# Kernel tuning notes

Hardware: AMD Instinct MI355X
Metric: run time of the kernel (lower is better)

Reference implementation:

```python
import jax, jax.numpy as jnp
import numpy as np
import math

HIDDEN = 1024
HEADS = 16
HEAD_DIM = HIDDEN // HEADS


def setup_inputs() -> dict:
    key = jax.random.key(0)
    ks = jax.random.split(key, 9)
    s = 1.0 / math.sqrt(HIDDEN)
    x = jax.random.normal(ks[0], (4, 2048, HIDDEN), dtype=jnp.float32)
    Wq = jax.random.uniform(ks[1], (HIDDEN, HIDDEN), jnp.float32, -s, s)
    bq = jax.random.uniform(ks[2], (HIDDEN,), jnp.float32, -s, s)
    Wk = jax.random.uniform(ks[3], (HIDDEN, HIDDEN), jnp.float32, -s, s)
    bk = jax.random.uniform(ks[4], (HIDDEN,), jnp.float32, -s, s)
    Wv = jax.random.uniform(ks[5], (HIDDEN, HIDDEN), jnp.float32, -s, s)
    bv = jax.random.uniform(ks[6], (HIDDEN,), jnp.float32, -s, s)
    Wo = jax.random.uniform(ks[7], (HIDDEN, HIDDEN), jnp.float32, -s, s)
    bo = jax.random.uniform(ks[8], (HIDDEN,), jnp.float32, -s, s)
    return {"x": x, "Wq": Wq, "bq": bq, "Wk": Wk, "bk": bk,
            "Wv": Wv, "bv": bv, "Wo": Wo, "bo": bo}


def reference(x, Wq, bq, Wk, bk, Wv, bv, Wo, bo):
    B, T, D = x.shape
    H, Hd = HEADS, HEAD_DIM
    scale = 1.0 / math.sqrt(Hd)
    # projections (torch Linear: y = x @ W.T + b)
    q = (x @ Wq.T + bq).reshape(B, T, H, Hd).transpose(0, 2, 1, 3)  # [B,H,T,Hd]
    k = (x @ Wk.T + bk).reshape(B, T, H, Hd).transpose(0, 2, 1, 3)
    v = (x @ Wv.T + bv).reshape(B, T, H, Hd).transpose(0, 2, 1, 3)
    scores = jnp.einsum("bhqd,bhkd->bhqk", q, k) * scale  # [B,H,T,T]
    attn = jax.nn.softmax(scores, axis=-1)
    out = jnp.einsum("bhqk,bhkd->bhqd", attn, v)  # [B,H,T,Hd]
    out = out.transpose(0, 2, 1, 3).reshape(B, T, D)
    out = out @ Wo.T + bo
    return out.mean(axis=1)  # [B, D]
```

## Files before the change

### kernel.cpp

```cpp
#include <hip/hip_runtime.h>
#include <stdint.h>

#define HIDDEN 1024
#define HEADS 16
#define HEAD_DIM 64
#define BATCH 4
#define SEQ 2048
#define NTOK (BATCH * SEQ)

typedef __attribute__((ext_vector_type(8))) short bf16x8;
typedef __attribute__((ext_vector_type(4))) float floatx4;
typedef __attribute__((ext_vector_type(16))) float floatx16;

#define SCALE_Q 0.18033688011112042f

__device__ __forceinline__ unsigned short f2bf(float f) {
    union { float f; unsigned u; } x; x.f = f;
    unsigned r = x.u + 0x7fffu + ((x.u >> 16) & 1u);
    return (unsigned short)(r >> 16);
}

__device__ __forceinline__ float fast_exp2(float x) {
#if __has_builtin(__builtin_amdgcn_exp2f)
    return __builtin_amdgcn_exp2f(x);
#else
    return exp2f(x);
#endif
}

typedef __attribute__((address_space(3))) unsigned int lds_u32;
typedef const __attribute__((address_space(1))) unsigned int gl_u32;

__device__ __forceinline__ void async_cp16(const void* g, void* l) {
#if __has_builtin(__builtin_amdgcn_global_load_lds)
    __builtin_amdgcn_global_load_lds((gl_u32*)g, (lds_u32*)l, 16, 0, 0);
#else
    *(uint4*)((char*)l + (threadIdx.x & 63) * 16) = *(const uint4*)g;
#endif
}

__global__ __launch_bounds__(256) void conv_all(
    const float* __restrict__ x, const float* __restrict__ Wq,
    const float* __restrict__ Wk, const float* __restrict__ Wv,
    unsigned short* __restrict__ x_bf, unsigned short* __restrict__ wq_bf,
    unsigned short* __restrict__ wk_bf, unsigned short* __restrict__ wv_bf,
    float* __restrict__ accp) {
    const int blk = blockIdx.x, tid = threadIdx.x;
    const float* src;
    unsigned short* dst;
    size_t i;
    if (blk < 8192) {
        src = x; dst = x_bf; i = (size_t)blk * 256 + tid;
        if (blk < 16) accp[blk * 256 + tid] = 0.0f;
    } else {
        int r = blk - 8192;
        int s = r >> 10;
        src = (s == 0) ? Wq : (s == 1) ? Wk : Wv;
        dst = (s == 0) ? wq_bf : (s == 1) ? wk_bf : wv_bf;
        i = (size_t)(r & 1023) * 256 + tid;
    }
    float4 v = *(const float4*)(src + 4 * i);
    unsigned short o[4];
    o[0] = f2bf(v.x); o[1] = f2bf(v.y); o[2] = f2bf(v.z); o[3] = f2bf(v.w);
    *(ushort4*)(dst + 4 * i) = *(ushort4*)o;
}

__global__ __launch_bounds__(256, 3) void qkv_gemm(
    const unsigned short* __restrict__ X,
    const unsigned short* __restrict__ W0, const unsigned short* __restrict__ W1,
    const unsigned short* __restrict__ W2,
    const float* __restrict__ b0, const float* __restrict__ b1,
    const float* __restrict__ b2,
    unsigned short* __restrict__ O0, unsigned short* __restrict__ O1,
    unsigned short* __restrict__ O2) {
    __shared__ unsigned short Alds[2][4096];
    __shared__ unsigned short Blds[2][4096];

    const int id = blockIdx.x;
    const int y = id >> 6;
    const int z = y >> 3;
    const int n0 = (y & 7) * 128;
    const int m0 = (id & 63) * 128;
    const unsigned short* W = (z == 0) ? W0 : (z == 1) ? W1 : W2;
    const float* bias       = (z == 0) ? b0 : (z == 1) ? b1 : b2;
    unsigned short* O       = (z == 0) ? O0 : (z == 1) ? O1 : O2;

    const int tid = threadIdx.x, lane = tid & 63, wave = tid >> 6;
    const int mw = (wave >> 1) * 64, nw = (wave & 1) * 64;

    const int sr = lane >> 2;
    const int scb = (lane & 3) * 8;
    const unsigned short* ga[2];
    const unsigned short* gb[2];
#pragma unroll
    for (int j = 0; j < 2; ++j) {
        ga[j] = X + (size_t)(m0 + wave * 32 + j * 16 + sr) * HIDDEN + scb;
        gb[j] = W + (size_t)(n0 + wave * 32 + j * 16 + sr) * HIDDEN + scb;
    }

    floatx4 acc[4][4];
#pragma unroll
    for (int tm = 0; tm < 4; ++tm)
#pragma unroll
        for (int tn = 0; tn < 4; ++tn)
#pragma unroll
            for (int r = 0; r < 4; ++r) acc[tm][tn][r] = 0.f;

#pragma unroll
    for (int j = 0; j < 2; ++j) {
        async_cp16(ga[j], (char*)Alds[0] + wave * 2048 + j * 1024);
        async_cp16(gb[j], (char*)Blds[0] + wave * 2048 + j * 1024);
        ga[j] += 32; gb[j] += 32;
    }
    __syncthreads();

    const int frag_off = (lane & 15) * 64 + (lane >> 4) * 16;
    for (int kt = 0; kt < 32; ++kt) {
        const int cur = kt & 1;
        if (kt < 31) {
#pragma unroll
            for (int j = 0; j < 2; ++j) {
                async_cp16(ga[j], (char*)Alds[cur ^ 1] + wave * 2048 + j * 1024);
                async_cp16(gb[j], (char*)Blds[cur ^ 1] + wave * 2048 + j * 1024);
                ga[j] += 32; gb[j] += 32;
            }
        }
        bf16x8 af[4], bfr[4];
#pragma unroll
        for (int t = 0; t < 4; ++t) {
            af[t]  = *(bf16x8*)((char*)Alds[cur] + (mw + t * 16) * 64 + frag_off);
            bfr[t] = *(bf16x8*)((char*)Blds[cur] + (nw + t * 16) * 64 + frag_off);
        }
#pragma unroll
        for (int tm = 0; tm < 4; ++tm)
#pragma unroll
            for (int tn = 0; tn < 4; ++tn)
                acc[tm][tn] = __builtin_amdgcn_mfma_f32_16x16x32_bf16(af[tm], bfr[tn], acc[tm][tn], 0, 0, 0);
        if (kt < 31) __syncthreads();
    }

    const int col = lane & 15, rbase = (lane >> 4) * 4;
#pragma unroll
    for (int tm = 0; tm < 4; ++tm) {
#pragma unroll
        for (int tn = 0; tn < 4; ++tn) {
            const int n = n0 + nw + tn * 16 + col;
            const float bs = bias[n];
            const int m_base = m0 + mw + tm * 16 + rbase;
            if (z == 2) {
                const int hh = n >> 6, dd = n & 63;
                const int bb = m_base >> 11, tt = m_base & (SEQ - 1);
                unsigned short vals[4];
#pragma unroll
                for (int r = 0; r < 4; ++r) vals[r] = f2bf(acc[tm][tn][r] + bs);
                *(ushort4*)&O[(((size_t)bb * HEADS + hh) * HEAD_DIM + dd) * SEQ + tt] = *(ushort4*)vals;
            } else {
                const float sc = (z == 0) ? SCALE_Q : 1.0f;
#pragma unroll
                for (int r = 0; r < 4; ++r)
                    O[(size_t)(m_base + r) * HIDDEN + n] = f2bf((acc[tm][tn][r] + bs) * sc);
            }
        }
    }
}

__global__ __launch_bounds__(256, 2) void attn_mfma(
    const unsigned short* __restrict__ Q, const unsigned short* __restrict__ K,
    const unsigned short* __restrict__ Vt, float* __restrict__ accp) {
    __shared__ unsigned short Klds[2][8192];
    __shared__ unsigned short Vlds[2][8192];

    const int tid = threadIdx.x, lane = tid & 63, wave = tid >> 6;
    const int lq = lane & 31, g2 = lane >> 5;

    const int f = blockIdx.x;
    const int bh = (f & 7) * 8 + ((f >> 3) & 7);
    const int qc = f >> 6;
    const int b = bh >> 4, h = bh & 15;

    bf16x8 qfrag[2][4];
#pragma unroll
    for (int g = 0; g < 2; ++g) {
        const size_t qb = ((size_t)(b * SEQ + qc * 256 + wave * 64 + g * 32 + lq)) * HIDDEN
                          + h * HEAD_DIM + g2 * 8;
#pragma unroll
        for (int ds = 0; ds < 4; ++ds) qfrag[g][ds] = *(const bf16x8*)&Q[qb + ds * 16];
    }

    const unsigned short* kg[4];
    const unsigned short* vg[4];
    {
        const int kr = lane >> 3;
        const int kc = ((lane & 7) ^ kr) * 8;
#pragma unroll
        for (int j = 0; j < 4; ++j)
            kg[j] = K + ((size_t)(b * SEQ + wave * 32 + j * 8 + kr)) * HIDDEN + h * HEAD_DIM + kc;
#pragma unroll
        for (int j = 0; j < 4; ++j) {
            const int dl = wave * 16 + j * 4 + (lane >> 4);
            const int cc = ((lane & 15) ^ (dl & 15)) * 8;
            vg[j] = Vt + ((size_t)bh * HEAD_DIM + dl) * SEQ + cc;
        }
    }

    floatx16 oacc[2][2], lacc[2];
#pragma unroll
    for (int g = 0; g < 2; ++g)
#pragma unroll
        for (int r = 0; r < 16; ++r) { oacc[g][0][r] = 0.f; oacc[g][1][r] = 0.f; lacc[g][r] = 0.f; }

    bf16x8 ones;
    {
        union { bf16x8 v; unsigned u[4]; } o;
        o.u[0] = o.u[1] = o.u[2] = o.u[3] = 0x3F803F80u;
        ones = o.v;
    }

#pragma unroll
    for (int j = 0; j < 4; ++j) {
        async_cp16(kg[j], (char*)Klds[0] + (wave * 32 + j * 8) * 128);
        async_cp16(vg[j], (char*)Vlds[0] + (wave * 16 + j * 4) * 256);
        kg[j] += 128 * HIDDEN; vg[j] += 128;
    }
    __syncthreads();

    for (int it = 0; it < 16; ++it) {
        const int cur = it & 1;
        if (it < 15) {
#pragma unroll
            for (int j = 0; j < 4; ++j) {
                async_cp16(kg[j], (char*)Klds[cur ^ 1] + (wave * 32 + j * 8) * 128);
                async_cp16(vg[j], (char*)Vlds[cur ^ 1] + (wave * 16 + j * 4) * 256);
                kg[j] += 128 * HIDDEN; vg[j] += 128;
            }
        }
#pragma unroll
        for (int ks4 = 0; ks4 < 4; ++ks4) {
            const int kk = ks4 * 32;
            const int rr = kk + lq;
            bf16x8 kf[4];
#pragma unroll
            for (int ds = 0; ds < 4; ++ds)
                kf[ds] = *(bf16x8*)((char*)Klds[cur] + rr * 128 + (((g2 + 2 * ds) ^ (lq & 7)) * 16));

            unsigned pk[2][8];
#pragma unroll
            for (int g = 0; g < 2; ++g) {
                floatx16 sacc;
#pragma unroll
                for (int r = 0; r < 16; ++r) sacc[r] = 0.f;
#pragma unroll
                for (int ds = 0; ds < 4; ++ds)
                    sacc = __builtin_amdgcn_mfma_f32_32x32x16_bf16(kf[ds], qfrag[g][ds], sacc, 0, 0, 0);
#pragma unroll
                for (int j = 0; j < 8; ++j) {
                    union { float f; unsigned u; } plo, phi;
                    plo.f = fast_exp2(sacc[2 * j]);
                    phi.f = fast_exp2(sacc[2 * j + 1]);
                    pk[g][j] = __builtin_amdgcn_perm(phi.u, plo.u, 0x07060302u);
                }
            }
#pragma unroll
            for (int ks2 = 0; ks2 < 2; ++ks2) {
                bf16x8 vf[2];
#pragma unroll
                for (int nf = 0; nf < 2; ++nf) {
                    const int d = nf * 32 + lq;
                    const int c0 = (4 * ks4 + 2 * ks2) ^ (d & 15);
                    const int c1 = (4 * ks4 + 2 * ks2 + 1) ^ (d & 15);
                    union { uint2 h[2]; bf16x8 v; } u;
                    u.h[0] = *(uint2*)((char*)Vlds[cur] + d * 256 + c0 * 16 + g2 * 8);
                    u.h[1] = *(uint2*)((char*)Vlds[cur] + d * 256 + c1 * 16 + g2 * 8);
                    vf[nf] = u.v;
                }
#pragma unroll
                for (int g = 0; g < 2; ++g) {
                    union { uint4 u; bf16x8 v; } af;
                    af.u.x = pk[g][4 * ks2];
                    af.u.y = pk[g][4 * ks2 + 1];
                    af.u.z = pk[g][4 * ks2 + 2];
                    af.u.w = pk[g][4 * ks2 + 3];
#pragma unroll
                    for (int nf = 0; nf < 2; ++nf)
                        oacc[g][nf] = __builtin_amdgcn_mfma_f32_32x32x16_bf16(af.v, vf[nf], oacc[g][nf], 0, 0, 0);
                    lacc[g] = __builtin_amdgcn_mfma_f32_32x32x16_bf16(af.v, ones, lacc[g], 0, 0, 0);
                }
            }
        }
        if (it < 15) __syncthreads();
    }

#pragma unroll
    for (int g = 0; g < 2; ++g)
#pragma unroll
        for (int nf = 0; nf < 2; ++nf) {
            float v = 0.f;
#pragma unroll
            for (int r = 0; r < 16; ++r) v += oacc[g][nf][r] / lacc[g][r];
            v += __shfl_xor(v, 32, 64);
            if (lane < 32)
                atomicAdd(&accp[b * HIDDEN + h * HEAD_DIM + nf * 32 + lq], v);
        }
}

__global__ __launch_bounds__(256) void out_proj(const float* __restrict__ acc,
                                                const float* __restrict__ Wo,
                                                const float* __restrict__ bo,
                                                float* __restrict__ out) {
    const int n = blockIdx.x * 256 + threadIdx.x;
    const int b = blockIdx.y;
    const float invT = 1.0f / (float)SEQ;
    float s = 0.f;
    for (int k = 0; k < HIDDEN; k += 4) {
        float4 w = *(const float4*)&Wo[(size_t)n * HIDDEN + k];
        float4 a = *(const float4*)&acc[b * HIDDEN + k];
        s += w.x * a.x + w.y * a.y + w.z * a.z + w.w * a.w;
    }
    out[b * HIDDEN + n] = s * invT + bo[n];
}

extern "C" void kernel_launch(void* const* d_in, const int* in_sizes, int n_in,
                              void* d_out, int out_size, void* d_ws, size_t ws_size,
                              hipStream_t stream) {
    const float* x  = (const float*)d_in[0];
    const float* Wq = (const float*)d_in[1];
    const float* bq = (const float*)d_in[2];
    const float* Wk = (const float*)d_in[3];
    const float* bk = (const float*)d_in[4];
    const float* Wv = (const float*)d_in[5];
    const float* bv = (const float*)d_in[6];
    const float* Wo = (const float*)d_in[7];
    const float* bo = (const float*)d_in[8];
    float* out = (float*)d_out;

    char* ws = (char*)d_ws;
    unsigned short* x_bf  = (unsigned short*)(ws);
    unsigned short* wq_bf = (unsigned short*)(ws + 16777216);
    unsigned short* wk_bf = (unsigned short*)(ws + 18874368);
    unsigned short* wv_bf = (unsigned short*)(ws + 20971520);
    unsigned short* q_bf  = (unsigned short*)(ws + 23068672);
    unsigned short* k_bf  = (unsigned short*)(ws + 39845888);
    unsigned short* vt_bf = (unsigned short*)(ws + 56623104);
    float*          accp  = (float*)(ws + 73400320);

    conv_all<<<dim3(8192 + 3072), dim3(256), 0, stream>>>(
        x, Wq, Wk, Wv, x_bf, wq_bf, wk_bf, wv_bf, accp);

    qkv_gemm<<<dim3(64 * 24), dim3(256), 0, stream>>>(
        x_bf, wq_bf, wk_bf, wv_bf, bq, bk, bv, q_bf, k_bf, vt_bf);

    attn_mfma<<<dim3(512), dim3(256), 0, stream>>>(q_bf, k_bf, vt_bf, accp);

    out_proj<<<dim3(HIDDEN / 256, BATCH), dim3(256), 0, stream>>>(accp, Wo, bo, out);
}
```

Before: 266.2 us.

## Swizzle GEMM LDS, stage epilogue through shared memory, split out_proj reduction

The QKV GEMM now XOR-swizzles the LDS tile layout to cut bank conflicts on fragment loads. Its epilogue stages results through a padded shared tile so Q/K/V^T are written with coalesced 16-byte stores, replacing scattered 2-byte stores and the strided transposed V writes. The out_proj kernel splits the K dimension across four waves with a shared-memory reduction, giving more blocks and shorter per-thread loops. The costs are extra LDS use, which may lower occupancy, and additional barriers.

```diff
diff --git a/kernel.cpp b/kernel.cpp
--- a/kernel.cpp
+++ b/kernel.cpp
@@ -73,29 +73,27 @@
     const float* __restrict__ b2,
     unsigned short* __restrict__ O0, unsigned short* __restrict__ O1,
     unsigned short* __restrict__ O2) {
-    __shared__ unsigned short Alds[2][4096];
-    __shared__ unsigned short Blds[2][4096];
+    __shared__ __align__(16) char smem[34816];
+    unsigned short* tbuf = (unsigned short*)smem;
 
     const int id = blockIdx.x;
-    const int y = id >> 6;
-    const int z = y >> 3;
-    const int n0 = (y & 7) * 128;
-    const int m0 = (id & 63) * 128;
+    const int mb = id & 63, nzb = id >> 6;
+    const int z = nzb >> 3, nz = nzb & 7;
+    const int m0 = mb * 128;
     const unsigned short* W = (z == 0) ? W0 : (z == 1) ? W1 : W2;
     const float* bias       = (z == 0) ? b0 : (z == 1) ? b1 : b2;
-    unsigned short* O       = (z == 0) ? O0 : (z == 1) ? O1 : O2;
 
     const int tid = threadIdx.x, lane = tid & 63, wave = tid >> 6;
-    const int mw = (wave >> 1) * 64, nw = (wave & 1) * 64;
-
-    const int sr = lane >> 2;
-    const int scb = (lane & 3) * 8;
+    const int wm = (wave & 1) * 64, wn = (wave >> 1) * 64;
+
+    const int srow = lane >> 2;
+    const int sxc = ((lane & 3) ^ (srow & 3)) * 8;
     const unsigned short* ga[2];
     const unsigned short* gb[2];
 #pragma unroll
     for (int j = 0; j < 2; ++j) {
-        ga[j] = X + (size_t)(m0 + wave * 32 + j * 16 + sr) * HIDDEN + scb;
-        gb[j] = W + (size_t)(n0 + wave * 32 + j * 16 + sr) * HIDDEN + scb;
+        ga[j] = X + (size_t)(m0 + wave * 32 + j * 16 + srow) * HIDDEN + sxc;
+        gb[j] = W + (size_t)(nz * 128 + wave * 32 + j * 16 + srow) * HIDDEN + sxc;
     }
 
     floatx4 acc[4][4];
@@ -108,28 +106,30 @@
 
 #pragma unroll
     for (int j = 0; j < 2; ++j) {
-        async_cp16(ga[j], (char*)Alds[0] + wave * 2048 + j * 1024);
-        async_cp16(gb[j], (char*)Blds[0] + wave * 2048 + j * 1024);
+        async_cp16(ga[j], smem + wave * 2048 + j * 1024);
+        async_cp16(gb[j], smem + 16384 + wave * 2048 + j * 1024);
         ga[j] += 32; gb[j] += 32;
     }
     __syncthreads();
 
-    const int frag_off = (lane & 15) * 64 + (lane >> 4) * 16;
+    const int fr = (lane & 15) * 64 + (((lane >> 4) ^ (lane & 3)) * 16);
     for (int kt = 0; kt < 32; ++kt) {
         const int cur = kt & 1;
         if (kt < 31) {
 #pragma unroll
             for (int j = 0; j < 2; ++j) {
-                async_cp16(ga[j], (char*)Alds[cur ^ 1] + wave * 2048 + j * 1024);
-                async_cp16(gb[j], (char*)Blds[cur ^ 1] + wave * 2048 + j * 1024);
+                async_cp16(ga[j], smem + (cur ^ 1) * 8192 + wave * 2048 + j * 1024);
+                async_cp16(gb[j], smem + 16384 + (cur ^ 1) * 8192 + wave * 2048 + j * 1024);
                 ga[j] += 32; gb[j] += 32;
             }
         }
+        const char* Ab = smem + cur * 8192;
+        const char* Bb = smem + 16384 + cur * 8192;
         bf16x8 af[4], bfr[4];
 #pragma unroll
         for (int t = 0; t < 4; ++t) {
-            af[t]  = *(bf16x8*)((char*)Alds[cur] + (mw + t * 16) * 64 + frag_off);
-            bfr[t] = *(bf16x8*)((char*)Blds[cur] + (nw + t * 16) * 64 + frag_off);
+            af[t]  = *(bf16x8*)(Ab + (wm + t * 16) * 64 + fr);
+            bfr[t] = *(bf16x8*)(Bb + (wn + t * 16) * 64 + fr);
         }
 #pragma unroll
         for (int tm = 0; tm < 4; ++tm)
@@ -140,27 +140,51 @@
     }
 
     const int col = lane & 15, rbase = (lane >> 4) * 4;
-#pragma unroll
-    for (int tm = 0; tm < 4; ++tm) {
-#pragma unroll
-        for (int tn = 0; tn < 4; ++tn) {
-            const int n = n0 + nw + tn * 16 + col;
-            const float bs = bias[n];
-            const int m_base = m0 + mw + tm * 16 + rbase;
-            if (z == 2) {
-                const int hh = n >> 6, dd = n & 63;
-                const int bb = m_base >> 11, tt = m_base & (SEQ - 1);
+    __syncthreads();
+    if (z == 2) {
+#pragma unroll
+        for (int tm = 0; tm < 4; ++tm)
+#pragma unroll
+            for (int tn = 0; tn < 4; ++tn) {
+                const int dr = wn + tn * 16 + col;
+                const float bs = bias[nz * 128 + dr];
+                const int mi0 = wm + tm * 16 + rbase;
                 unsigned short vals[4];
 #pragma unroll
                 for (int r = 0; r < 4; ++r) vals[r] = f2bf(acc[tm][tn][r] + bs);
-                *(ushort4*)&O[(((size_t)bb * HEADS + hh) * HEAD_DIM + dd) * SEQ + tt] = *(ushort4*)vals;
-            } else {
-                const float sc = (z == 0) ? SCALE_Q : 1.0f;
+                *(ushort4*)&tbuf[dr * 136 + mi0] = *(ushort4*)vals;
+            }
+        __syncthreads();
+        const int dr = tid >> 1, seg = tid & 1;
+        const int hh = nz * 2 + (dr >> 6), dd = dr & 63;
+        const int bb = m0 >> 11, tb = (m0 & (SEQ - 1)) >> 7;
+        unsigned short* dst = O2 + (((size_t)bb * HEADS + hh) * HEAD_DIM + dd) * SEQ
+                                 + tb * 128 + seg * 64;
+        const unsigned short* srcl = &tbuf[dr * 136 + seg * 64];
+#pragma unroll
+        for (int i = 0; i < 8; ++i)
+            *(uint4*)(dst + i * 8) = *(const uint4*)(srcl + i * 8);
+    } else {
+        unsigned short* O = (z == 0) ? O0 : O1;
+        const float sc = (z == 0) ? SCALE_Q : 1.0f;
+#pragma unroll
+        for (int tm = 0; tm < 4; ++tm)
+#pragma unroll
+            for (int tn = 0; tn < 4; ++tn) {
+                const int nn = wn + tn * 16 + col;
+                const float bs = bias[nz * 128 + nn];
+                const int mi0 = wm + tm * 16 + rbase;
 #pragma unroll
                 for (int r = 0; r < 4; ++r)
-                    O[(size_t)(m_base + r) * HIDDEN + n] = f2bf((acc[tm][tn][r] + bs) * sc);
-            }
-        }
+                    tbuf[(mi0 + r) * 136 + nn] = f2bf((acc[tm][tn][r] + bs) * sc);
+            }
+        __syncthreads();
+        const int r = tid >> 1, seg = tid & 1;
+        unsigned short* dst = O + (size_t)(m0 + r) * HIDDEN + nz * 128 + seg * 64;
+        const unsigned short* srcl = &tbuf[r * 136 + seg * 64];
+#pragma unroll
+        for (int i = 0; i < 8; ++i)
+            *(uint4*)(dst + i * 8) = *(const uint4*)(srcl + i * 8);
     }
 }
 
@@ -307,16 +331,26 @@
                                                 const float* __restrict__ Wo,
                                                 const float* __restrict__ bo,
                                                 float* __restrict__ out) {
-    const int n = blockIdx.x * 256 + threadIdx.x;
+    __shared__ float red[256];
+    const int n = blockIdx.x * 64 + (threadIdx.x & 63);
+    const int ks = threadIdx.x >> 6;
     const int b = blockIdx.y;
-    const float invT = 1.0f / (float)SEQ;
+    const float* wr = Wo + (size_t)n * HIDDEN + ks * 256;
+    const float* ar = acc + b * HIDDEN + ks * 256;
     float s = 0.f;
-    for (int k = 0; k < HIDDEN; k += 4) {
-        float4 w = *(const float4*)&Wo[(size_t)n * HIDDEN + k];
-        float4 a = *(const float4*)&acc[b * HIDDEN + k];
+#pragma unroll 8
+    for (int k = 0; k < 256; k += 4) {
+        float4 w = *(const float4*)(wr + k);
+        float4 a = *(const float4*)(ar + k);
         s += w.x * a.x + w.y * a.y + w.z * a.z + w.w * a.w;
     }
-    out[b * HIDDEN + n] = s * invT + bo[n];
+    red[threadIdx.x] = s;
+    __syncthreads();
+    if (threadIdx.x < 64) {
+        float t = red[threadIdx.x] + red[threadIdx.x + 64]
+                + red[threadIdx.x + 128] + red[threadIdx.x + 192];
+        out[b * HIDDEN + n] = t * (1.0f / (float)SEQ) + bo[n];
+    }
 }
 
 extern "C" void kernel_launch(void* const* d_in, const int* in_sizes, int n_in,
@@ -346,10 +380,10 @@
     conv_all<<<dim3(8192 + 3072), dim3(256), 0, stream>>>(
         x, Wq, Wk, Wv, x_bf, wq_bf, wk_bf, wv_bf, accp);
 
-    qkv_gemm<<<dim3(64 * 24), dim3(256), 0, stream>>>(
+    qkv_gemm<<<dim3(1536), dim3(256), 0, stream>>>(
         x_bf, wq_bf, wk_bf, wv_bf, bq, bk, bv, q_bf, k_bf, vt_bf);
 
     attn_mfma<<<dim3(512), dim3(256), 0, stream>>>(q_bf, k_bf, vt_bf, accp);
 
-    out_proj<<<dim3(HIDDEN / 256, BATCH), dim3(256), 0, stream>>>(accp, Wo, bo, out);
-}
+    out_proj<<<dim3(16, BATCH), dim3(256), 0, stream>>>(accp, Wo, bo, out);
+}
```

Result: faster. 255.4 us (-4.0%).
